# Kernel optimization log

Hardware: AMD Instinct MI355X
Metric: run time of the kernel (lower is better)

The kernel has to match this reference:

```python
import jax, jax.numpy as jnp
import numpy as np
from functools import partial

# Config (BranchNet 'big'-style)
HIST = [42, 78, 150, 294, 582]
PW = [3, 6, 12, 24, 48]
SHIFTING = [False, False, True, True, True]
CW = 7          # conv width
F = 32          # conv filters
E = 32          # embedding dims
B = 4096        # batch
H_TOT = 590     # total history length
V = 8192        # 2**(pc_hash_bits+1)
WBITS = 2       # weight quantization bits
ABITS = 3       # activation quantization bits
EPS = 1e-5


@partial(jax.custom_vjp, nondiff_argnums=(1,))
def quant_signed(x, bits):
    # Quantize.forward (signed, bits>1): round(x*scale)/scale, scale=(1<<(bits-1))-1
    scale = float((1 << (bits - 1)) - 1)
    return jnp.round(x * scale) / scale

def _q_fwd(x, bits):
    return quant_signed(x, bits), None

def _q_bwd(bits, res, g):
    # straight-through estimator, matching Quantize.backward
    return (g,)

quant_signed.defvjp(_q_fwd, _q_bwd)


def batchnorm(x, gamma, beta, axes, pshape):
    # training-mode BatchNorm1d: batch statistics, biased variance
    m = jnp.mean(x, axis=axes, keepdims=True)
    v = jnp.var(x, axis=axes, keepdims=True)
    return gamma.reshape(pshape) * (x - m) * jax.lax.rsqrt(v + EPS) + beta.reshape(pshape)


def extract_slice_history(x, global_shift, slice_size, pooling_width, shifting):
    # vectorized version of the per-sample Python loop in extract_slice_history
    h_tot = x.shape[1]
    if shifting:
        s = jnp.mod(global_shift, pooling_width)              # [B]
        start = (h_tot - s - slice_size)[:, None]             # [B,1]
        idx = start + jnp.arange(slice_size)[None, :]         # [B,L]
        return jnp.take_along_axis(x, idx, axis=1)
    return x[:, -slice_size:]


def fc_layer(x, W, b, gamma, beta):
    # FCLayer with quantized weights + batchnorm + hardtanh + quantized act
    w = quant_signed(jnp.clip(W, -1.0, 1.0), WBITS)
    y = x @ w.T + b
    y = batchnorm(y, gamma, beta, (0,), (1, -1))
    y = jnp.clip(y, -1.0, 1.0)  # hardtanh
    return quant_signed(y, ABITS)


def branchnet_forward(x, global_shift, emb, conv_w, conv_b, bn1_g, bn1_b,
                      bnp_g, bnp_b, W1, b1, g1, be1, W2, b2, g2, be2, W3, b3):
    feats = []
    for i in range(len(HIST)):
        L, pw = HIST[i], PW[i]
        xs = extract_slice_history(x, global_shift, L, pw, SHIFTING[i])  # [B,L] int
        e = jnp.take(emb[i], xs, axis=0)                                 # [B,L,E]
        e = jnp.transpose(e, (0, 2, 1))                                  # [B,E,L]
        h = jax.lax.conv_general_dilated(
            e, conv_w[i], window_strides=(1,), padding='VALID',
            dimension_numbers=('NCH', 'OIH', 'NCH')) + conv_b[i][None, :, None]
        h = batchnorm(h, bn1_g[i], bn1_b[i], (0, 2), (1, -1, 1))
        h = jnp.tanh(h)
        T = (L - CW + 1) // pw                                           # = 12
        p = h[:, :, :T * pw].reshape(h.shape[0], F, T, pw).mean(axis=-1) # AvgPool1d
        p = batchnorm(p, bnp_g[i], bnp_b[i], (0, 2), (1, -1, 1))
        feats.append(p.reshape(p.shape[0], -1))                          # [B, F*T]
    z = jnp.concatenate(feats, axis=1)                                   # [B, 1920]
    z = fc_layer(z, W1, b1, g1, be1)
    z = fc_layer(z, W2, b2, g2, be2)
    w3 = quant_signed(jnp.clip(W3, -1.0, 1.0), WBITS)
    out = z @ w3.T + b3                                                  # [B,1]
    return out[:, 0]                                                     # squeeze(dim=1)


def setup_inputs() -> dict:
    key = jax.random.key(0)
    ks = jax.random.split(key, 12)
    return {
        'x': jax.random.randint(ks[0], (B, H_TOT), 0, V, dtype=jnp.int32),
        'global_shift': jax.random.randint(ks[1], (B,), 0, 48, dtype=jnp.int32),
        'emb': jax.random.normal(ks[2], (5, V, E), jnp.float32) * 0.1,
        'conv_w': jax.random.normal(ks[3], (5, F, E, CW), jnp.float32) * 0.1,
        'conv_b': jax.random.normal(ks[4], (5, F), jnp.float32) * 0.01,
        'bn1_g': jnp.ones((5, F), jnp.float32),
        'bn1_b': jnp.zeros((5, F), jnp.float32),
        'bnp_g': jnp.ones((5, F), jnp.float32),
        'bnp_b': jnp.zeros((5, F), jnp.float32),
        'W1': jax.random.uniform(ks[5], (2048, 1920), jnp.float32, -1.0, 1.0),
        'b1': jax.random.normal(ks[6], (2048,), jnp.float32) * 0.01,
        'g1': jnp.ones((2048,), jnp.float32),
        'be1': jnp.zeros((2048,), jnp.float32),
        'W2': jax.random.uniform(ks[7], (2048, 2048), jnp.float32, -1.0, 1.0),
        'b2': jax.random.normal(ks[8], (2048,), jnp.float32) * 0.01,
        'g2': jnp.ones((2048,), jnp.float32),
        'be2': jnp.zeros((2048,), jnp.float32),
        'W3': jax.random.uniform(ks[9], (1, 2048), jnp.float32, -1.0, 1.0),
        'b3': jax.random.normal(ks[10], (1,), jnp.float32) * 0.01,
    }


def reference(x, global_shift, emb, conv_w, conv_b, bn1_g, bn1_b, bnp_g, bnp_b,
              W1, b1, g1, be1, W2, b2, g2, be2, W3, b3):
    return branchnet_forward(x, global_shift, emb, conv_w, conv_b, bn1_g, bn1_b,
                             bnp_g, bnp_b, W1, b1, g1, be1, W2, b2, g2, be2, W3, b3)
```

## Files before the change

### kernel.cpp

```cpp
#include <hip/hip_runtime.h>
#include <cmath>

#define HTOT  590
#define BATCH 4096
#define VOCAB 8192

typedef _Float16 f16;
typedef __attribute__((ext_vector_type(8))) _Float16 f16x8;
typedef __attribute__((ext_vector_type(4))) _Float16 f16x4;
typedef __attribute__((ext_vector_type(4))) float f32x4;
typedef __attribute__((ext_vector_type(16))) float f32x16;

constexpr size_t OFF_EHL  = 0;
constexpr size_t OFF_WF   = 1310720;
constexpr size_t OFF_PA   = 1347584;
constexpr size_t OFF_PB   = 2921472;
constexpr size_t OFF_BN1  = 4494336;
constexpr size_t OFF_BNP  = 4494656;
constexpr size_t OFF_CP   = 4494976;
constexpr size_t OFF_BNF1 = 4626048;
constexpr size_t OFF_PRAW = 4630528;
constexpr size_t OFF_W1P  = 12494848;
constexpr size_t OFF_W2P  = 14460928;
constexpr size_t OFF_Y    = 16558080;
constexpr size_t OFF_BNF2 = 24946688;
constexpr size_t OFF_Z2K  = 0;
constexpr size_t OFF_Z3K  = 4194304;
constexpr size_t OFF_H    = 24950784;
constexpr size_t END_H    = 180140032;

__device__ __forceinline__ float qw(float w) {
  return rintf(fminf(fmaxf(w, -1.f), 1.f));
}
__device__ __forceinline__ float4 ld4(const float* p) {
  return *reinterpret_cast<const float4*>(p);
}
__device__ __forceinline__ float tanh_c(float u) {
  const float e = __expf(2.f*u);
  return 1.f - __fdividef(2.f, e + 1.f);
}

#define MF(A,B,C) __builtin_amdgcn_mfma_f32_32x32x16_f16(A,B,C,0,0,0)

__global__ __launch_bounds__(256) void k_eprep(const float* __restrict__ emb,
                                               f16* __restrict__ ehl)
{
  const int idx = blockIdx.x*256 + threadIdx.x;
  const int c = idx & 31, v = (idx >> 5) & 8191, slice = idx >> 18;
  const float val = emb[(size_t)(slice*VOCAB + v)*32 + c];
  const f16 hi = (f16)val;
  const f16 lo = (f16)((val - (float)hi)*2048.f);
  f16* row = ehl + (size_t)(slice*VOCAB + v)*64;
  row[c] = hi; row[32 + c] = lo;
}

__global__ __launch_bounds__(256) void k_wfprep(const float* __restrict__ convw,
                                                f16* __restrict__ wf)
{
  const int idx = blockIdx.x*256 + threadIdx.x;
  const int j = idx & 7, lane = (idx >> 3) & 63, hl = (idx >> 9) & 1, ks = (idx >> 10) & 1;
  const int kk = idx >> 11, k = kk % 7, slice = kk / 7;
  const int f = lane & 31, c = ks*16 + (lane >> 5)*8 + j;
  const float val = convw[((slice*32 + f)*32 + c)*7 + k];
  const f16 hi = (f16)val;
  wf[idx] = hl ? (f16)((val - (float)hi)*2048.f) : hi;
}

template<int PASS, int H>
__global__ __launch_bounds__(256, 3) void k_convm(const int* __restrict__ x,
                                                  const int* __restrict__ gshift,
                                                  const float* __restrict__ ehl,
                                                  const float* __restrict__ wfrag,
                                                  const float* __restrict__ bn1,
                                                  float* __restrict__ z,
                                                  float* __restrict__ partials,
                                                  unsigned* __restrict__ hbuf)
{
  const int b = blockIdx.x;
  const int type = blockIdx.y;
  const int tid = threadIdx.x;
  const int wid = tid >> 6, lane = tid & 63;
  const int lt = lane & 31, hf = lane >> 5;

  __shared__ float smem[10584];
  __shared__ int   tokid[294];

  float* tokrow = smem;
  float* thbuf  = smem;
  float* poolb  = smem + 4224;
  f16*   hstat  = (f16*)smem;
  float* part2  = smem + 6000;

  const int gsv = gshift[b];
  const int NTOK = (type == 0) ? 270 : 294;

  if (!(PASS == 1 && H == 1)) {
    for (int i = tid; i < NTOK; i += 256) {
      int xs, q = i;
      if (type == 0) {
        if (i < 42)       { xs = 548; }
        else if (i < 120) { xs = 512; q = i - 42; }
        else              { xs = 440 - gsv % 12; q = i - 120; }
      } else if (type == 1) xs = 296 - gsv % 24;
      else if (type == 2)   xs = 8 - gsv % 48;
      else                  xs = 8 - gsv % 48 + 288;
      int xi = xs + q; if (xi < 0) xi += HTOT;
      tokid[i] = x[b*HTOT + xi];
    }
    __syncthreads();
    for (int j = tid; j < NTOK*8; j += 256) {
      const int row = j >> 3, ch = j & 7;
      const int sl = (type == 0) ? (row < 42 ? 0 : (row < 120 ? 1 : 2)) : ((type == 1) ? 3 : 4);
      const float4 v = ld4(ehl + (size_t)(sl*VOCAB + tokid[row])*32 + ch*4);
      *reinterpret_cast<float4*>(&tokrow[row*36 + ch*4]) = v;
    }
    __syncthreads();
  }

  int slice, tb, nt, slotoff, ThV, pw, si;
  if (type == 0) {
    if      (wid == 0) { slice=0; tb=0;  nt=2; slotoff=0;   ThV=36;  pw=3;  si=0; }
    else if (wid == 1) { slice=1; tb=0;  nt=3; slotoff=42;  ThV=72;  pw=6;  si=1; }
    else if (wid == 2) { slice=2; tb=0;  nt=3; slotoff=120; ThV=144; pw=12; si=2; }
    else               { slice=2; tb=96; nt=2; slotoff=120; ThV=144; pw=12; si=2; }
  } else if (type == 1) {
    slice=3; pw=24; ThV=288; slotoff=0; si=0;
    tb = (wid == 0) ? 0 : 32 + wid*64; nt = (wid == 0) ? 3 : 2;
  } else if (type == 2) {
    slice=4; pw=48; ThV=288; slotoff=0; si=0;
    tb = (wid == 0) ? 0 : 32 + wid*64; nt = (wid == 0) ? 3 : 2;
  } else {
    slice=4; pw=48; ThV=576; slotoff=-288; si=0;
    tb = 288 + ((wid == 0) ? 0 : 32 + wid*64); nt = (wid == 0) ? 3 : 2;
  }
  const int wb = (type == 3) ? 6 : 0;
  const int slot0 = (type == 0) ? ((wid == 0) ? 0 : (wid == 1) ? 2 : (wid == 2) ? 5 : 8)
                                : ((wid == 0) ? 0 : 1 + wid*2);
  const int tbase = (type == 0) ? 0 : 10 + (type - 1)*9;

  const float* wfsl = wfrag + slice*7168;
  #define LDA(K,KS,HL) (*reinterpret_cast<const f16x8*>(wfsl + (((K)*2+(KS))*2+(HL))*256 + lane*4))

  f32x16 a0[3], a1[3];

  if (!(PASS == 1 && H == 1)) {
    #pragma unroll
    for (int r = 0; r < 3; ++r) {
      #pragma unroll
      for (int i = 0; i < 16; ++i) { a0[r][i] = 0.f; a1[r][i] = 0.f; }
    }
    const float* pb = tokrow + (size_t)(slotoff + tb + lt)*36 + hf*4;
    #pragma unroll
    for (int k = 0; k < 7; ++k) {
      const f16x8 wh0 = LDA(k,0,0), wl0 = LDA(k,0,1), wh1 = LDA(k,1,0), wl1 = LDA(k,1,1);
      #pragma unroll
      for (int r = 0; r < 3; ++r) if (r < nt) {
        const float* rp = pb + k*36 + r*1152;
        const f16x8 bh0 = *(const f16x8*)(rp),    bh1 = *(const f16x8*)(rp+8);
        const f16x8 bl0 = *(const f16x8*)(rp+16), bl1 = *(const f16x8*)(rp+24);
        a0[r]=MF(wh0,bh0,a0[r]); a1[r]=MF(wh0,bl0,a1[r]); a1[r]=MF(wl0,bh0,a1[r]);
        a0[r]=MF(wh1,bh1,a0[r]); a1[r]=MF(wh1,bl1,a1[r]); a1[r]=MF(wl1,bh1,a1[r]);
      }
    }
    __syncthreads();
  }

  if (PASS == 0) {
    #pragma unroll
    for (int r = 0; r < 3; ++r) if (r < nt) {
      const int tbg = tb + r*32;
      const int slot = slot0 + r;
      unsigned* hd = H ? (hbuf + ((size_t)b*37 + tbase + slot)*1024 + lt) : nullptr;
      #pragma unroll
      for (int i = 0; i < 16; ++i) {
        const int fr = (i&3) + 8*(i>>2) + 4*hf;
        const float h = a0[r][i] + a1[r][i]*(1.f/2048.f);
        if (H) {
          const f16 hi = (f16)h;
          const f16 lo = (f16)((h - (float)hi)*2048.f);
          hd[fr*32] = (unsigned)__builtin_bit_cast(unsigned short, hi)
                    | ((unsigned)__builtin_bit_cast(unsigned short, lo) << 16);
        }
        const float hv = (tbg + lt < ThV) ? h : 0.f;
        hstat[slot*1088 + fr*34 + lt] = (f16)hv;
      }
    }
    __syncthreads();
    const int nslot = (type == 0) ? 10 : 9;
    for (int j = tid; j < nslot*32; j += 256) {
      const int slot = j >> 5, f = j & 31;
      const f16* rowp = hstat + slot*1088 + f*34;
      float s1 = 0.f, s2 = 0.f;
      #pragma unroll
      for (int t = 0; t < 32; ++t) { const float v = (float)rowp[t]; s1 += v; s2 += v*v; }
      part2[(slot*32 + f)*2]     = s1;
      part2[(slot*32 + f)*2 + 1] = s2;
    }
    __syncthreads();
    const int nch = (type == 0) ? 96 : 32;
    if (tid < nch) {
      const int sic = tid >> 5, f = tid & 31;
      int slo, shi, Pb;
      if (type == 0) {
        slo = (sic == 0) ? 0 : (sic == 1) ? 2 : 5;
        shi = (sic == 0) ? 2 : (sic == 1) ? 5 : 10;
        Pb  = sic*32;
      } else { slo = 0; shi = 9; Pb = 96 + (type - 1)*32; }
      float s1 = 0.f, s2 = 0.f;
      for (int s = slo; s < shi; ++s) {
        s1 += part2[(s*32 + f)*2];
        s2 += part2[(s*32 + f)*2 + 1];
      }
      partials[(size_t)b*384 + (Pb + f)*2]     = s1;
      partials[(size_t)b*384 + (Pb + f)*2 + 1] = s2;
    }
    return;
  }

  for (int i = tid; i < 2304; i += 256) poolb[i] = 0.f;
  __syncthreads();

  float A1v[16], B1v[16];
  #pragma unroll
  for (int i = 0; i < 16; ++i) {
    const int fr = (i&3) + 8*(i>>2) + 4*hf;
    A1v[i] = bn1[slice*32 + fr];
    B1v[i] = bn1[160 + slice*32 + fr];
  }

  #pragma unroll
  for (int r = 0; r < 3; ++r) if (r < nt) {
    const int tbg = tb + r*32;
    const unsigned* hs = H ? (hbuf + ((size_t)b*37 + tbase + slot0 + r)*1024 + lt) : nullptr;
    #pragma unroll
    for (int i = 0; i < 16; ++i) {
      const int fr = (i&3) + 8*(i>>2) + 4*hf;
      float h;
      if (H) {
        const unsigned w = hs[fr*32];
        const f16 hi = __builtin_bit_cast(f16, (unsigned short)(w & 0xffffu));
        const f16 lo = __builtin_bit_cast(f16, (unsigned short)(w >> 16));
        h = (float)hi + (float)lo*(1.f/2048.f);
      } else {
        h = a0[r][i] + a1[r][i]*(1.f/2048.f);
      }
      thbuf[wid*1056 + fr*33 + lt] = tanh_c(A1v[i]*h + B1v[i]);
    }
    const int tvend = min(tbg + 32, ThV);
    const int wlo = tbg / pw, whi = (tvend - 1) / pw;
    for (int w = wlo; w <= whi; ++w) {
      const int lo = max(w*pw, tbg), hi2 = min((w+1)*pw, tvend);
      float s = 0.f;
      for (int t = lo + hf; t < hi2; t += 2) s += thbuf[wid*1056 + lt*33 + (t - tbg)];
      s += __shfl_xor(s, 32);
      if (hf == 0) {
        const int piece = (w*pw < tbg) ? 1 : 0;
        poolb[(si*12 + (w - wb))*64 + piece*32 + lt] = s;
      }
    }
  }
  __syncthreads();

  const int nch = (type == 0) ? 96 : 32;
  if (tid < nch) {
    const int sic = tid >> 5, f = tid & 31;
    const int sg = (type == 0) ? sic : ((type == 1) ? 3 : 4);
    const int P = (sg < 4) ? sg*32 + f : ((type == 2) ? 128 + f : 160 + f);
    const int pwc = (type == 0) ? ((sic == 0) ? 3 : (sic == 1) ? 6 : 12)
                                : ((type == 1) ? 24 : 48);
    const int nwin = (type >= 2) ? 6 : 12;
    const int wbc = (type == 3) ? 6 : 0;
    const float inv = 1.f/(float)pwc;
    float s1 = 0.f, s2 = 0.f;
    for (int wl = 0; wl < nwin; ++wl) {
      const float p = (poolb[(sic*12 + wl)*64 + f] + poolb[(sic*12 + wl)*64 + 32 + f]) * inv;
      z[(size_t)b*1920 + sg*384 + (wl + wbc)*32 + f] = p;
      s1 += p; s2 += p*p;
    }
    partials[(size_t)b*384 + P*2]     = s1;
    partials[(size_t)b*384 + P*2 + 1] = s2;
  }
}

template<int PASS>
__global__ __launch_bounds__(256) void k_bnfinal(const float* __restrict__ partials,
                                                 const float* __restrict__ gamma,
                                                 const float* __restrict__ beta,
                                                 float* __restrict__ outAB)
{
  const int c = blockIdx.x;
  const int slice = c >> 5, f = c & 31;
  const int tid = threadIdx.x;
  double s1 = 0.0, s2 = 0.0;
  for (int b = tid; b < BATCH; b += 256) {
    const float* p = partials + (size_t)b*384;
    if (slice < 4) { s1 += p[(slice*32+f)*2]; s2 += p[(slice*32+f)*2+1]; }
    else {
      s1 += (double)p[(128+f)*2]   + (double)p[(160+f)*2];
      s2 += (double)p[(128+f)*2+1] + (double)p[(160+f)*2+1];
    }
  }
  __shared__ double r1[256], r2[256];
  r1[tid] = s1; r2[tid] = s2;
  __syncthreads();
  for (int off = 128; off > 0; off >>= 1) {
    if (tid < off) { r1[tid] += r1[tid+off]; r2[tid] += r2[tid+off]; }
    __syncthreads();
  }
  if (tid == 0) {
    long N;
    if (PASS == 0) { const long Tall[5] = {36,72,144,288,576}; N = (long)BATCH * Tall[slice]; }
    else           { N = (long)BATCH * 12; }
    const double m   = r1[0]/(double)N;
    const double var = r2[0]/(double)N - m*m;
    const float rstd = (float)(1.0/sqrt(var + 1e-5));
    const float Aa = gamma[c]*rstd;
    outAB[c]       = Aa;
    outAB[160 + c] = beta[c] - Aa*(float)m;
  }
}

__global__ __launch_bounds__(256) void k_znorm(float* __restrict__ zz,
                                               const float* __restrict__ bnp)
{
  const size_t i4 = (size_t)blockIdx.x*256 + threadIdx.x;
  const float4 v = ld4(zz + i4*4);
  const int j = (int)((i4*4) % 1920);
  const int slice = j / 384, f0 = j & 31;
  const float4 A = ld4(bnp + slice*32 + f0);
  const float4 B = ld4(bnp + 160 + slice*32 + f0);
  const float zn[4] = {v.x*A.x+B.x, v.y*A.y+B.y, v.z*A.z+B.z, v.w*A.w+B.w};
  uint4 pk;
  unsigned w[4];
  #pragma unroll
  for (int e = 0; e < 4; ++e) {
    const f16 hi = (f16)zn[e];
    const f16 lo = (f16)(zn[e] - (float)hi);
    w[e] = (unsigned)__builtin_bit_cast(unsigned short, hi)
         | ((unsigned)__builtin_bit_cast(unsigned short, lo) << 16);
  }
  pk.x = w[0]; pk.y = w[1]; pk.z = w[2]; pk.w = w[3];
  *reinterpret_cast<uint4*>(zz + i4*4) = pk;
}

__global__ __launch_bounds__(256) void k_wprep1(const float* __restrict__ W1,
                                                f16* __restrict__ W1p)
{
  const int idx = blockIdx.x*256 + threadIdx.x;
  const int n = idx / 1920, klds = idx - n*1920;
  const int slice = klds / 384, r = klds - slice*384;
  const int tp = r >> 5, f = r & 31;
  W1p[idx] = (f16)qw(W1[n*1920 + slice*384 + f*12 + tp]);
}

__global__ __launch_bounds__(256) void k_wprep2(const float* __restrict__ W2,
                                                f16* __restrict__ W2p)
{
  const size_t i4 = (size_t)blockIdx.x*256 + threadIdx.x;
  const float4 v = ld4(W2 + i4*4);
  f16x4 o;
  o[0] = (f16)qw(v.x); o[1] = (f16)qw(v.y); o[2] = (f16)qw(v.z); o[3] = (f16)qw(v.w);
  *reinterpret_cast<f16x4*>(&W2p[i4*4]) = o;
}

template<int SPLIT, int PACKED>
__global__ __launch_bounds__(256) void k_mfgemm(const f16* __restrict__ Ahi,
                                               const unsigned* __restrict__ Apk,
                                               const f16* __restrict__ Bp,
                                               float* __restrict__ C,
                                               const int K, const float oscale)
{
  __shared__ f16 sA[(SPLIT+1)*128][40];
  __shared__ f16 sB[128][40];
  const int tid = threadIdx.x;
  const int bm = blockIdx.y*128, bn = blockIdx.x*128;
  const int wid = tid >> 6, lane = tid & 63;
  const int wm = (wid >> 1)*64, wn = (wid & 1)*64;
  const int lgrp = lane >> 4, lrow = lane & 15;
  f32x4 acc[4][4];
  #pragma unroll
  for (int m = 0; m < 4; ++m)
    #pragma unroll
    for (int n = 0; n < 4; ++n) acc[m][n] = (f32x4){0.f,0.f,0.f,0.f};

  const int srow = tid >> 2, sc = (tid & 3)*8;
  for (int k0 = 0; k0 < K; k0 += 32) {
    #pragma unroll
    for (int u = 0; u < 2; ++u) {
      const int row = srow + u*64;
      if (PACKED) {
        const unsigned* ap = Apk + (size_t)(bm+row)*K + k0 + sc;
        const uint4 v0 = *reinterpret_cast<const uint4*>(ap);
        const uint4 v1 = *reinterpret_cast<const uint4*>(ap + 4);
        uint4 hi, lo;
        hi.x = (v0.x & 0xffffu) | (v0.y << 16);  hi.y = (v0.z & 0xffffu) | (v0.w << 16);
        hi.z = (v1.x & 0xffffu) | (v1.y << 16);  hi.w = (v1.z & 0xffffu) | (v1.w << 16);
        lo.x = (v0.x >> 16) | (v0.y & 0xffff0000u);  lo.y = (v0.z >> 16) | (v0.w & 0xffff0000u);
        lo.z = (v1.x >> 16) | (v1.y & 0xffff0000u);  lo.w = (v1.z >> 16) | (v1.w & 0xffff0000u);
        *reinterpret_cast<uint4*>(&sA[row][sc])     = hi;
        *reinterpret_cast<uint4*>(&sA[128+row][sc]) = lo;
      } else {
        const uint4 va = *reinterpret_cast<const uint4*>(&Ahi[(size_t)(bm+row)*K + k0 + sc]);
        *reinterpret_cast<uint4*>(&sA[row][sc]) = va;
      }
      const uint4 vb = *reinterpret_cast<const uint4*>(&Bp[(size_t)(bn+row)*K + k0 + sc]);
      *reinterpret_cast<uint4*>(&sB[row][sc]) = vb;
    }
    __syncthreads();
    f16x8 bf[4];
    #pragma unroll
    for (int n = 0; n < 4; ++n)
      bf[n] = *reinterpret_cast<const f16x8*>(&sB[wn + n*16 + lrow][lgrp*8]);
    #pragma unroll
    for (int m = 0; m < 4; ++m) {
      const f16x8 ah = *reinterpret_cast<const f16x8*>(&sA[wm + m*16 + lrow][lgrp*8]);
      #pragma unroll
      for (int n = 0; n < 4; ++n)
        acc[m][n] = __builtin_amdgcn_mfma_f32_16x16x32_f16(ah, bf[n], acc[m][n], 0, 0, 0);
      if (SPLIT) {
        const f16x8 al = *reinterpret_cast<const f16x8*>(&sA[128 + wm + m*16 + lrow][lgrp*8]);
        #pragma unroll
        for (int n = 0; n < 4; ++n)
          acc[m][n] = __builtin_amdgcn_mfma_f32_16x16x32_f16(al, bf[n], acc[m][n], 0, 0, 0);
      }
    }
    __syncthreads();
  }
  #pragma unroll
  for (int m = 0; m < 4; ++m)
    #pragma unroll
    for (int n = 0; n < 4; ++n) {
      const int col = bn + wn + n*16 + lrow;
      #pragma unroll
      for (int r = 0; r < 4; ++r)
        C[(size_t)(bm + wm + m*16 + lgrp*4 + r)*2048 + col] = acc[m][n][r]*oscale;
    }
}

__global__ __launch_bounds__(256) void k_colpart(const float* __restrict__ Y,
                                                 double* __restrict__ part, int N)
{
  const int c0 = blockIdx.x*64;
  const int chunk = blockIdx.y;
  const int tid = threadIdx.x;
  const int c = tid & 63, rq = tid >> 6;
  double s1 = 0.0, s2 = 0.0;
  const int rbase = chunk*256;
  for (int r = rbase + rq; r < rbase+256; r += 4) {
    const float v = Y[(size_t)r*N + c0 + c];
    s1 += (double)v; s2 += (double)v*(double)v;
  }
  __shared__ double r1[256], r2[256];
  r1[tid] = s1; r2[tid] = s2;
  __syncthreads();
  if (tid < 64) {
    const double a  = r1[tid]+r1[tid+64]+r1[tid+128]+r1[tid+192];
    const double cc = r2[tid]+r2[tid+64]+r2[tid+128]+r2[tid+192];
    part[(size_t)(c0+c)*32 + chunk*2]     = a;
    part[(size_t)(c0+c)*32 + chunk*2 + 1] = cc;
  }
}

__global__ __launch_bounds__(256) void k_colfinal(const double* __restrict__ part,
                                                  const float* __restrict__ gamma,
                                                  const float* __restrict__ beta,
                                                  float* __restrict__ bnfc, int N)
{
  const int c = blockIdx.x*256 + threadIdx.x;
  if (c >= N) return;
  double s1 = 0.0, s2 = 0.0;
  #pragma unroll
  for (int ch = 0; ch < 16; ++ch) {
    s1 += part[(size_t)c*32 + ch*2];
    s2 += part[(size_t)c*32 + ch*2 + 1];
  }
  const double m   = s1/4096.0;
  const double var = s2/4096.0 - m*m;
  const float rstd = (float)(1.0/sqrt(var + 1e-5));
  const float Aa = gamma[c]*rstd;
  bnfc[c]        = Aa;
  bnfc[2048 + c] = beta[c] - Aa*(float)m;
}

__global__ __launch_bounds__(256) void k_act(const float* __restrict__ Y,
                                             const float* __restrict__ bnfc,
                                             f16* __restrict__ Zk)
{
  const size_t i4 = (size_t)blockIdx.x*256 + threadIdx.x;
  const int cbase = (int)((i4*4) & 2047);
  const float4 v = ld4(Y + i4*4);
  const float4 A = ld4(bnfc + cbase);
  const float4 B = ld4(bnfc + 2048 + cbase);
  const float t[4] = {v.x*A.x+B.x, v.y*A.y+B.y, v.z*A.z+B.z, v.w*A.w+B.w};
  f16x4 o;
  #pragma unroll
  for (int e = 0; e < 4; ++e) {
    const float c = fminf(fmaxf(t[e], -1.f), 1.f);
    o[e] = (f16)rintf(c*3.f);
  }
  *reinterpret_cast<f16x4*>(&Zk[i4*4]) = o;
}

__global__ __launch_bounds__(256) void k_final(const f16* __restrict__ Z3,
                                               const float* __restrict__ W3,
                                               const float* __restrict__ b3,
                                               float* __restrict__ out)
{
  const int b = blockIdx.x;
  const int tid = threadIdx.x;
  float s = 0.f;
  for (int j = tid; j < 2048; j += 256)
    s += (float)Z3[(size_t)b*2048 + j] * qw(W3[j]);
  __shared__ float red[256];
  red[tid] = s;
  __syncthreads();
  for (int off = 128; off > 0; off >>= 1) {
    if (tid < off) red[tid] += red[tid+off];
    __syncthreads();
  }
  if (tid == 0) out[b] = red[0]*(1.f/3.f) + b3[0];
}

extern "C" void kernel_launch(void* const* d_in, const int* in_sizes, int n_in,
                              void* d_out, int out_size, void* d_ws, size_t ws_size,
                              hipStream_t stream)
{
  const int*   x    = (const int*)d_in[0];
  const int*   gs   = (const int*)d_in[1];
  const float* emb  = (const float*)d_in[2];
  const float* cw   = (const float*)d_in[3];
  const float* bn1g = (const float*)d_in[5];
  const float* bn1b = (const float*)d_in[6];
  const float* bnpg = (const float*)d_in[7];
  const float* bnpb = (const float*)d_in[8];
  const float* W1   = (const float*)d_in[9];
  const float* g1   = (const float*)d_in[11];
  const float* be1  = (const float*)d_in[12];
  const float* W2   = (const float*)d_in[13];
  const float* g2   = (const float*)d_in[15];
  const float* be2  = (const float*)d_in[16];
  const float* W3   = (const float*)d_in[17];
  const float* b3   = (const float*)d_in[18];
  float* ws  = (float*)d_ws;
  float* out = (float*)d_out;

  const bool useH = ws_size >= (size_t)END_H * 4ull;
  unsigned* hbuf = (unsigned*)(ws + OFF_H);

  k_eprep<<<5120, 256, 0, stream>>>(emb, (f16*)(ws + OFF_EHL));
  k_wfprep<<<280, 256, 0, stream>>>(cw, (f16*)(ws + OFF_WF));

  if (useH) {
    k_convm<0,1><<<dim3(BATCH, 4), 256, 0, stream>>>(x, gs, ws + OFF_EHL, ws + OFF_WF,
                                                     ws + OFF_BN1, nullptr, ws + OFF_PA, hbuf);
    k_bnfinal<0><<<160, 256, 0, stream>>>(ws + OFF_PA, bn1g, bn1b, ws + OFF_BN1);
    k_convm<1,1><<<dim3(BATCH, 4), 256, 0, stream>>>(x, gs, ws + OFF_EHL, ws + OFF_WF,
                                                     ws + OFF_BN1, ws + OFF_PRAW, ws + OFF_PB, hbuf);
  } else {
    k_convm<0,0><<<dim3(BATCH, 4), 256, 0, stream>>>(x, gs, ws + OFF_EHL, ws + OFF_WF,
                                                     ws + OFF_BN1, nullptr, ws + OFF_PA, hbuf);
    k_bnfinal<0><<<160, 256, 0, stream>>>(ws + OFF_PA, bn1g, bn1b, ws + OFF_BN1);
    k_convm<1,0><<<dim3(BATCH, 4), 256, 0, stream>>>(x, gs, ws + OFF_EHL, ws + OFF_WF,
                                                     ws + OFF_BN1, ws + OFF_PRAW, ws + OFF_PB, hbuf);
  }
  k_bnfinal<1><<<160, 256, 0, stream>>>(ws + OFF_PB, bnpg, bnpb, ws + OFF_BNP);
  k_znorm<<<7680, 256, 0, stream>>>(ws + OFF_PRAW, ws + OFF_BNP);
  k_wprep1<<<15360, 256, 0, stream>>>(W1, (f16*)(ws + OFF_W1P));
  k_wprep2<<<4096, 256, 0, stream>>>(W2, (f16*)(ws + OFF_W2P));

  k_mfgemm<1,1><<<dim3(16, 32), 256, 0, stream>>>(nullptr, (const unsigned*)(ws + OFF_PRAW),
                                                  (const f16*)(ws + OFF_W1P),
                                                  ws + OFF_Y, 1920, 1.f);
  k_colpart<<<dim3(32, 16), 256, 0, stream>>>(ws + OFF_Y, (double*)(ws + OFF_CP), 2048);
  k_colfinal<<<8, 256, 0, stream>>>((const double*)(ws + OFF_CP), g1, be1, ws + OFF_BNF1, 2048);
  k_act<<<8192, 256, 0, stream>>>(ws + OFF_Y, ws + OFF_BNF1, (f16*)(ws + OFF_Z2K));

  k_mfgemm<0,0><<<dim3(16, 32), 256, 0, stream>>>((const f16*)(ws + OFF_Z2K), nullptr,
                                                  (const f16*)(ws + OFF_W2P),
                                                  ws + OFF_Y, 2048, 1.f/3.f);
  k_colpart<<<dim3(32, 16), 256, 0, stream>>>(ws + OFF_Y, (double*)(ws + OFF_CP), 2048);
  k_colfinal<<<8, 256, 0, stream>>>((const double*)(ws + OFF_CP), g2, be2, ws + OFF_BNF2, 2048);
  k_act<<<8192, 256, 0, stream>>>(ws + OFF_Y, ws + OFF_BNF2, (f16*)(ws + OFF_Z3K));

  k_final<<<4096, 256, 0, stream>>>((const f16*)(ws + OFF_Z3K), W3, b3, out);
}
```

Baseline: 834.4 us.

## Recompute conv in both passes with single accumulator and channel-major token layout

```diff
diff --git a/kernel.cpp b/kernel.cpp
--- a/kernel.cpp
+++ b/kernel.cpp
@@ -13,21 +13,19 @@
 
 constexpr size_t OFF_EHL  = 0;
 constexpr size_t OFF_WF   = 1310720;
-constexpr size_t OFF_PA   = 1347584;
-constexpr size_t OFF_PB   = 2921472;
-constexpr size_t OFF_BN1  = 4494336;
-constexpr size_t OFF_BNP  = 4494656;
-constexpr size_t OFF_CP   = 4494976;
-constexpr size_t OFF_BNF1 = 4626048;
-constexpr size_t OFF_PRAW = 4630528;
-constexpr size_t OFF_W1P  = 12494848;
-constexpr size_t OFF_W2P  = 14460928;
-constexpr size_t OFF_Y    = 16558080;
-constexpr size_t OFF_BNF2 = 24946688;
+constexpr size_t OFF_PA   = 1364480;
+constexpr size_t OFF_PB   = 2937344;
+constexpr size_t OFF_BN1  = 4510208;
+constexpr size_t OFF_BNP  = 4510528;
+constexpr size_t OFF_CP   = 4510848;
+constexpr size_t OFF_BNF1 = 4641920;
+constexpr size_t OFF_PRAW = 4646016;
+constexpr size_t OFF_W1P  = 12510336;
+constexpr size_t OFF_W2P  = 14476416;
+constexpr size_t OFF_Y    = 16573568;
+constexpr size_t OFF_BNF2 = 24962176;
 constexpr size_t OFF_Z2K  = 0;
 constexpr size_t OFF_Z3K  = 4194304;
-constexpr size_t OFF_H    = 24950784;
-constexpr size_t END_H    = 180140032;
 
 __device__ __forceinline__ float qw(float w) {
   return rintf(fminf(fmaxf(w, -1.f), 1.f));
@@ -41,6 +39,7 @@
 }
 
 #define MF(A,B,C) __builtin_amdgcn_mfma_f32_32x32x16_f16(A,B,C,0,0,0)
+#define WV(K,KS,V) (*reinterpret_cast<const f16x8*>(wfsl + (((K)*2+(KS))*3+(V))*256 + lane*4))
 
 __global__ __launch_bounds__(256) void k_eprep(const float* __restrict__ emb,
                                                f16* __restrict__ ehl)
@@ -58,23 +57,30 @@
                                                 f16* __restrict__ wf)
 {
   const int idx = blockIdx.x*256 + threadIdx.x;
-  const int j = idx & 7, lane = (idx >> 3) & 63, hl = (idx >> 9) & 1, ks = (idx >> 10) & 1;
-  const int kk = idx >> 11, k = kk % 7, slice = kk / 7;
+  const int j = idx & 7, lane = (idx >> 3) & 63;
+  const int rest = idx >> 9;
+  const int v = rest % 3;
+  const int rest2 = rest / 3;
+  const int ks = rest2 & 1, kk = rest2 >> 1;
+  const int k = kk % 7, slice = kk / 7;
   const int f = lane & 31, c = ks*16 + (lane >> 5)*8 + j;
   const float val = convw[((slice*32 + f)*32 + c)*7 + k];
   const f16 hi = (f16)val;
-  wf[idx] = hl ? (f16)((val - (float)hi)*2048.f) : hi;
-}
-
-template<int PASS, int H>
-__global__ __launch_bounds__(256, 3) void k_convm(const int* __restrict__ x,
+  f16 o;
+  if (v == 0)      o = (f16)((float)hi * 2048.f);
+  else if (v == 1) o = (f16)((val - (float)hi)*2048.f);
+  else             o = hi;
+  wf[idx] = o;
+}
+
+template<int PASS>
+__global__ __launch_bounds__(256, 4) void k_convm(const int* __restrict__ x,
                                                   const int* __restrict__ gshift,
                                                   const float* __restrict__ ehl,
                                                   const float* __restrict__ wfrag,
                                                   const float* __restrict__ bn1,
                                                   float* __restrict__ z,
-                                                  float* __restrict__ partials,
-                                                  unsigned* __restrict__ hbuf)
+                                                  float* __restrict__ partials)
 {
   const int b = blockIdx.x;
   const int type = blockIdx.y;
@@ -82,40 +88,38 @@
   const int wid = tid >> 6, lane = tid & 63;
   const int lt = lane & 31, hf = lane >> 5;
 
-  __shared__ float smem[10584];
+  __shared__ float smem[9408];
   __shared__ int   tokid[294];
 
-  float* tokrow = smem;
+  float* tokarr = smem;
+  f16*   hstat  = (f16*)smem;
+  float* part2  = smem + 6000;
   float* thbuf  = smem;
   float* poolb  = smem + 4224;
-  f16*   hstat  = (f16*)smem;
-  float* part2  = smem + 6000;
 
   const int gsv = gshift[b];
   const int NTOK = (type == 0) ? 270 : 294;
 
-  if (!(PASS == 1 && H == 1)) {
-    for (int i = tid; i < NTOK; i += 256) {
-      int xs, q = i;
-      if (type == 0) {
-        if (i < 42)       { xs = 548; }
-        else if (i < 120) { xs = 512; q = i - 42; }
-        else              { xs = 440 - gsv % 12; q = i - 120; }
-      } else if (type == 1) xs = 296 - gsv % 24;
-      else if (type == 2)   xs = 8 - gsv % 48;
-      else                  xs = 8 - gsv % 48 + 288;
-      int xi = xs + q; if (xi < 0) xi += HTOT;
-      tokid[i] = x[b*HTOT + xi];
-    }
-    __syncthreads();
-    for (int j = tid; j < NTOK*8; j += 256) {
-      const int row = j >> 3, ch = j & 7;
-      const int sl = (type == 0) ? (row < 42 ? 0 : (row < 120 ? 1 : 2)) : ((type == 1) ? 3 : 4);
-      const float4 v = ld4(ehl + (size_t)(sl*VOCAB + tokid[row])*32 + ch*4);
-      *reinterpret_cast<float4*>(&tokrow[row*36 + ch*4]) = v;
-    }
-    __syncthreads();
-  }
+  for (int i = tid; i < NTOK; i += 256) {
+    int xs, q = i;
+    if (type == 0) {
+      if (i < 42)       { xs = 548; }
+      else if (i < 120) { xs = 512; q = i - 42; }
+      else              { xs = 440 - gsv % 12; q = i - 120; }
+    } else if (type == 1) xs = 296 - gsv % 24;
+    else if (type == 2)   xs = 8 - gsv % 48;
+    else                  xs = 8 - gsv % 48 + 288;
+    int xi = xs + q; if (xi < 0) xi += HTOT;
+    tokid[i] = x[b*HTOT + xi];
+  }
+  __syncthreads();
+  for (int j = tid; j < NTOK*8; j += 256) {
+    const int row = j >> 3, ch = j & 7;
+    const int sl = (type == 0) ? (row < 42 ? 0 : (row < 120 ? 1 : 2)) : ((type == 1) ? 3 : 4);
+    const float4 v = ld4(ehl + (size_t)(sl*VOCAB + tokid[row])*32 + ch*4);
+    *reinterpret_cast<float4*>(&tokarr[ch*1176 + row*4]) = v;
+  }
+  __syncthreads();
 
   int slice, tb, nt, slotoff, ThV, pw, si;
   if (type == 0) {
@@ -136,51 +140,46 @@
   const int wb = (type == 3) ? 6 : 0;
   const int slot0 = (type == 0) ? ((wid == 0) ? 0 : (wid == 1) ? 2 : (wid == 2) ? 5 : 8)
                                 : ((wid == 0) ? 0 : 1 + wid*2);
-  const int tbase = (type == 0) ? 0 : 10 + (type - 1)*9;
-
-  const float* wfsl = wfrag + slice*7168;
-  #define LDA(K,KS,HL) (*reinterpret_cast<const f16x8*>(wfsl + (((K)*2+(KS))*2+(HL))*256 + lane*4))
-
-  f32x16 a0[3], a1[3];
-
-  if (!(PASS == 1 && H == 1)) {
-    #pragma unroll
-    for (int r = 0; r < 3; ++r) {
-      #pragma unroll
-      for (int i = 0; i < 16; ++i) { a0[r][i] = 0.f; a1[r][i] = 0.f; }
-    }
-    const float* pb = tokrow + (size_t)(slotoff + tb + lt)*36 + hf*4;
-    #pragma unroll
-    for (int k = 0; k < 7; ++k) {
-      const f16x8 wh0 = LDA(k,0,0), wl0 = LDA(k,0,1), wh1 = LDA(k,1,0), wl1 = LDA(k,1,1);
-      #pragma unroll
-      for (int r = 0; r < 3; ++r) if (r < nt) {
-        const float* rp = pb + k*36 + r*1152;
-        const f16x8 bh0 = *(const f16x8*)(rp),    bh1 = *(const f16x8*)(rp+8);
-        const f16x8 bl0 = *(const f16x8*)(rp+16), bl1 = *(const f16x8*)(rp+24);
-        a0[r]=MF(wh0,bh0,a0[r]); a1[r]=MF(wh0,bl0,a1[r]); a1[r]=MF(wl0,bh0,a1[r]);
-        a0[r]=MF(wh1,bh1,a0[r]); a1[r]=MF(wh1,bl1,a1[r]); a1[r]=MF(wl1,bh1,a1[r]);
-      }
-    }
-    __syncthreads();
-  }
+
+  const float* wfsl = wfrag + slice*10752;
+
+  f32x16 acc[3];
+  #pragma unroll
+  for (int r = 0; r < 3; ++r)
+    #pragma unroll
+    for (int i = 0; i < 16; ++i) acc[r][i] = 0.f;
+
+  const float* pb = tokarr + hf*1176 + (size_t)(slotoff + tb + lt)*4;
+  #pragma unroll 1
+  for (int k = 0; k < 7; ++k) {
+    const f16x8 wh2_0 = WV(k,0,0), wl_0 = WV(k,0,1), wh_0 = WV(k,0,2);
+    const f16x8 wh2_1 = WV(k,1,0), wl_1 = WV(k,1,1), wh_1 = WV(k,1,2);
+    #pragma unroll
+    for (int r = 0; r < 3; ++r) if (r < nt) {
+      const float* rp = pb + k*4 + r*128;
+      const f16x8 bh0 = *(const f16x8*)(rp);
+      const f16x8 bh1 = *(const f16x8*)(rp + 2352);
+      const f16x8 bl0 = *(const f16x8*)(rp + 4704);
+      const f16x8 bl1 = *(const f16x8*)(rp + 7056);
+      acc[r] = MF(wh2_0, bh0, acc[r]);
+      acc[r] = MF(wl_0,  bh0, acc[r]);
+      acc[r] = MF(wh_0,  bl0, acc[r]);
+      acc[r] = MF(wh2_1, bh1, acc[r]);
+      acc[r] = MF(wl_1,  bh1, acc[r]);
+      acc[r] = MF(wh_1,  bl1, acc[r]);
+    }
+  }
+  __syncthreads();
 
   if (PASS == 0) {
     #pragma unroll
     for (int r = 0; r < 3; ++r) if (r < nt) {
       const int tbg = tb + r*32;
       const int slot = slot0 + r;
-      unsigned* hd = H ? (hbuf + ((size_t)b*37 + tbase + slot)*1024 + lt) : nullptr;
       #pragma unroll
       for (int i = 0; i < 16; ++i) {
         const int fr = (i&3) + 8*(i>>2) + 4*hf;
-        const float h = a0[r][i] + a1[r][i]*(1.f/2048.f);
-        if (H) {
-          const f16 hi = (f16)h;
-          const f16 lo = (f16)((h - (float)hi)*2048.f);
-          hd[fr*32] = (unsigned)__builtin_bit_cast(unsigned short, hi)
-                    | ((unsigned)__builtin_bit_cast(unsigned short, lo) << 16);
-        }
+        const float h = acc[r][i]*(1.f/2048.f);
         const float hv = (tbg + lt < ThV) ? h : 0.f;
         hstat[slot*1088 + fr*34 + lt] = (f16)hv;
       }
@@ -231,19 +230,10 @@
   #pragma unroll
   for (int r = 0; r < 3; ++r) if (r < nt) {
     const int tbg = tb + r*32;
-    const unsigned* hs = H ? (hbuf + ((size_t)b*37 + tbase + slot0 + r)*1024 + lt) : nullptr;
     #pragma unroll
     for (int i = 0; i < 16; ++i) {
       const int fr = (i&3) + 8*(i>>2) + 4*hf;
-      float h;
-      if (H) {
-        const unsigned w = hs[fr*32];
-        const f16 hi = __builtin_bit_cast(f16, (unsigned short)(w & 0xffffu));
-        const f16 lo = __builtin_bit_cast(f16, (unsigned short)(w >> 16));
-        h = (float)hi + (float)lo*(1.f/2048.f);
-      } else {
-        h = a0[r][i] + a1[r][i]*(1.f/2048.f);
-      }
+      const float h = acc[r][i]*(1.f/2048.f);
       thbuf[wid*1056 + fr*33 + lt] = tanh_c(A1v[i]*h + B1v[i]);
     }
     const int tvend = min(tbg + 32, ThV);
@@ -544,25 +534,14 @@
   float* ws  = (float*)d_ws;
   float* out = (float*)d_out;
 
-  const bool useH = ws_size >= (size_t)END_H * 4ull;
-  unsigned* hbuf = (unsigned*)(ws + OFF_H);
-
   k_eprep<<<5120, 256, 0, stream>>>(emb, (f16*)(ws + OFF_EHL));
-  k_wfprep<<<280, 256, 0, stream>>>(cw, (f16*)(ws + OFF_WF));
-
-  if (useH) {
-    k_convm<0,1><<<dim3(BATCH, 4), 256, 0, stream>>>(x, gs, ws + OFF_EHL, ws + OFF_WF,
-                                                     ws + OFF_BN1, nullptr, ws + OFF_PA, hbuf);
-    k_bnfinal<0><<<160, 256, 0, stream>>>(ws + OFF_PA, bn1g, bn1b, ws + OFF_BN1);
-    k_convm<1,1><<<dim3(BATCH, 4), 256, 0, stream>>>(x, gs, ws + OFF_EHL, ws + OFF_WF,
-                                                     ws + OFF_BN1, ws + OFF_PRAW, ws + OFF_PB, hbuf);
-  } else {
-    k_convm<0,0><<<dim3(BATCH, 4), 256, 0, stream>>>(x, gs, ws + OFF_EHL, ws + OFF_WF,
-                                                     ws + OFF_BN1, nullptr, ws + OFF_PA, hbuf);
-    k_bnfinal<0><<<160, 256, 0, stream>>>(ws + OFF_PA, bn1g, bn1b, ws + OFF_BN1);
-    k_convm<1,0><<<dim3(BATCH, 4), 256, 0, stream>>>(x, gs, ws + OFF_EHL, ws + OFF_WF,
-                                                     ws + OFF_BN1, ws + OFF_PRAW, ws + OFF_PB, hbuf);
-  }
+  k_wfprep<<<420, 256, 0, stream>>>(cw, (f16*)(ws + OFF_WF));
+
+  k_convm<0><<<dim3(BATCH, 4), 256, 0, stream>>>(x, gs, ws + OFF_EHL, ws + OFF_WF,
+                                                 ws + OFF_BN1, nullptr, ws + OFF_PA);
+  k_bnfinal<0><<<160, 256, 0, stream>>>(ws + OFF_PA, bn1g, bn1b, ws + OFF_BN1);
+  k_convm<1><<<dim3(BATCH, 4), 256, 0, stream>>>(x, gs, ws + OFF_EHL, ws + OFF_WF,
+                                                 ws + OFF_BN1, ws + OFF_PRAW, ws + OFF_PB);
   k_bnfinal<1><<<160, 256, 0, stream>>>(ws + OFF_PB, bnpg, bnpb, ws + OFF_BNP);
   k_znorm<<<7680, 256, 0, stream>>>(ws + OFF_PRAW, ws + OFF_BNP);
   k_wprep1<<<15360, 256, 0, stream>>>(W1, (f16*)(ws + OFF_W1P));
```

New measurement: 806.5 us. 1.03x faster.
